# Performance work log

Measured on AMD Instinct MI355X. Metric: run time of the kernel, lower is better.

Reference implementation:

```python
import jax, jax.numpy as jnp
import numpy as np

DIM = 512
HID = 128
OUT = 32
ORDER = 3
B, L = 4, 4096


def positional_encoding(seq_len, d):
    pos = jnp.arange(seq_len, dtype=jnp.float32)[:, None]
    div = jnp.exp(-jnp.log(jnp.float32(10000.0)) * jnp.arange(0, d, 2, dtype=jnp.float32) / d)
    ang = pos * div[None, :]  # [L, d/2]
    pe = jnp.zeros((seq_len, d), dtype=jnp.float32)
    pe = pe.at[:, 0::2].set(jnp.sin(ang))
    pe = pe.at[:, 1::2].set(jnp.cos(ang))
    return pe


def setup_inputs() -> dict:
    key = jax.random.key(0)
    ks = jax.random.split(key, 9)
    s = lambda fan_in: 1.0 / np.sqrt(fan_in)
    return {
        "u": jax.random.normal(ks[0], (B, L, DIM), dtype=jnp.float32),
        "pW": jax.random.uniform(ks[1], (DIM, DIM * (ORDER + 1)), jnp.float32, -s(DIM), s(DIM)),
        "pb": jax.random.uniform(ks[2], (DIM * (ORDER + 1),), jnp.float32, -s(DIM), s(DIM)),
        "cW": jax.random.uniform(ks[3], (DIM * (ORDER + 1), DIM * (ORDER + 1), 3), jnp.float32, -s(DIM * 4 * 3), s(DIM * 4 * 3)),
        "cb": jax.random.uniform(ks[4], (DIM * (ORDER + 1),), jnp.float32, -s(DIM * 4 * 3), s(DIM * 4 * 3)),
        "fW": jax.random.uniform(ks[5], (HID, ORDER * DIM), jnp.float32, -s(HID), s(HID)),
        "fb": jax.random.uniform(ks[6], (ORDER * DIM,), jnp.float32, -s(HID), s(HID)),
        "oW": jax.random.uniform(ks[7], (DIM, OUT), jnp.float32, -s(DIM), s(DIM)),
        "ob": jax.random.uniform(ks[8], (OUT,), jnp.float32, -s(DIM), s(DIM)),
    }


def _fft_conv(h_filter, v):
    # circular conv along seq dim: h_filter [L, D], v [B, L, D]
    Vf = jnp.fft.rfft(v, axis=1)
    Hf = jnp.fft.rfft(h_filter, axis=0)[None, :, :]
    return jnp.fft.irfft(Vf * Hf, n=v.shape[1], axis=1)


def reference(u, pW, pb, cW, cb, fW, fb, oW, ob):
    seq_len = u.shape[1]
    t = positional_encoding(seq_len, HID)  # [L, HID]
    # hann window, periodic=False
    n = jnp.arange(seq_len, dtype=jnp.float32)
    window = (0.5 * (1.0 - jnp.cos(2.0 * jnp.pi * n / (seq_len - 1))))[:, None]  # [L,1]

    hat_z = u @ pW + pb  # [B, L, 4*DIM]
    # conv1d over seq with kernel 3, padding 1, channels 4*DIM -> 4*DIM
    z = jax.lax.conv_general_dilated(
        hat_z.transpose(0, 2, 1), cW, window_strides=(1,), padding=[(1, 1)],
        dimension_numbers=("NCH", "OIH", "NCH"))
    z = (z + cb[None, :, None]).transpose(0, 2, 1)  # [B, L, 4*DIM]

    v = z[:, :, :DIM]
    projs = z[:, :, DIM:]  # [B, L, 3*DIM]

    hat_h = t @ fW + fb  # [L, 3*DIM]
    h = hat_h * window  # [L, 3*DIM]

    for k in range(ORDER):
        xn = projs[:, :, DIM * k:DIM * (k + 1)]
        hn = h[:, DIM * k:DIM * (k + 1)]
        v = xn * _fft_conv(hn, v)

    return v @ oW + ob  # [B, L, OUT]
```

## Files before the change

kernel.cpp:

```cpp
#include <hip/hip_runtime.h>

typedef __attribute__((ext_vector_type(8))) short short8;
typedef __attribute__((ext_vector_type(4))) float f32x4;
typedef __attribute__((ext_vector_type(4))) unsigned short ushort4v;
typedef unsigned short ushortT;

#define PADROWS 4098
#define HSTR 2056
#define PI_F 3.14159265358979323f
#define PHYS(i) ((i) ^ (((i) >> 4) & 15))

__device__ __forceinline__ ushortT f2bf(float f) {
  union { float f; unsigned int u; } v; v.f = f;
  unsigned int r = (v.u + 0x7FFFu + ((v.u >> 16) & 1u)) >> 16;
  return (ushortT)r;
}
__device__ __forceinline__ float bf2f(ushortT b) {
  union { unsigned int u; float f; } v; v.u = ((unsigned int)b) << 16;
  return v.f;
}

__device__ __forceinline__ void gl2lds16(const void* g, void* l) {
  __builtin_amdgcn_global_load_lds((const __attribute__((address_space(1))) void*)g,
                                   (__attribute__((address_space(3))) void*)l, 16, 0, 0);
}


__global__ void cast_flat(const float* __restrict__ in, ushortT* __restrict__ outb) {
  size_t idx = (size_t)blockIdx.x * 256 + threadIdx.x;
  f32x4 v = *(const f32x4*)(in + idx * 4);
  ushort4v r;
  r[0] = f2bf(v[0]); r[1] = f2bf(v[1]); r[2] = f2bf(v[2]); r[3] = f2bf(v[3]);
  *(ushort4v*)(outb + idx * 4) = r;
}

__global__ void convert_u_pad(const float* __restrict__ in, ushortT* __restrict__ up) {
  int blk = blockIdx.x;
  if (blk >= 8192) {
    int idx = (blk - 8192) * 256 + threadIdx.x;
    int col = idx & 511;
    int r = (idx >> 9) & 1;
    int b = idx >> 10;
    up[((size_t)b * PADROWS + (r ? 4097 : 0)) * 512 + col] = 0;
    return;
  }
  size_t idx = (size_t)blk * 256 + threadIdx.x;
  f32x4 v = *(const f32x4*)(in + idx * 4);
  ushort4v r;
  r[0] = f2bf(v[0]); r[1] = f2bf(v[1]); r[2] = f2bf(v[2]); r[3] = f2bf(v[3]);
  size_t g = idx * 4;
  int col = (int)(g & 511);
  int l = (int)(g >> 9);
  int b = l >> 12;
  *(ushort4v*)(up + ((size_t)b * PADROWS + (l & 4095) + 1) * 512 + col) = r;
}

__global__ void cwt_pbc(const float* __restrict__ cW, const float* __restrict__ pb,
                        const float* __restrict__ cb, ushortT* __restrict__ Wt,
                        float* __restrict__ biasC, float* __restrict__ pbC0,
                        float* __restrict__ pbC2) {
  int o = blockIdx.x;
  int tid = threadIdx.x;
  float s0 = 0.f, s1 = 0.f, s2 = 0.f;
  const float* base = cW + (size_t)o * 6144;
  for (int i = tid; i < 2048; i += 256) {
    float w0 = base[i * 3], w1 = base[i * 3 + 1], w2 = base[i * 3 + 2];
    size_t oi = (size_t)o * 2048 + i;
    Wt[oi]           = f2bf(w0);
    Wt[oi + 4194304] = f2bf(w1);
    Wt[oi + 8388608] = f2bf(w2);
    float p = pb[i];
    s0 = fmaf(p, w0, s0);
    s1 = fmaf(p, w1, s1);
    s2 = fmaf(p, w2, s2);
  }
#pragma unroll
  for (int off = 32; off >= 1; off >>= 1) {
    s0 += __shfl_down(s0, off);
    s1 += __shfl_down(s1, off);
    s2 += __shfl_down(s2, off);
  }
  __shared__ float red[4][3];
  if ((tid & 63) == 0) { red[tid >> 6][0] = s0; red[tid >> 6][1] = s1; red[tid >> 6][2] = s2; }
  __syncthreads();
  if (tid == 0) {
    float a0 = red[0][0] + red[1][0] + red[2][0] + red[3][0];
    float a1 = red[0][1] + red[1][1] + red[2][1] + red[3][1];
    float a2 = red[0][2] + red[1][2] + red[2][2] + red[3][2];
    biasC[o] = cb[o] + a0 + a1 + a2;
    pbC0[o] = a0;
    pbC2[o] = a2;
  }
}

__global__ void fill_tabs(float2* __restrict__ Wg, float2* __restrict__ Sg) {
  int m = blockIdx.x * 256 + threadIdx.x;
  float sn, cs;
  if (m < 2048) {
    sincosf(-2.0f * PI_F * (float)m / 2048.0f, &sn, &cs);
    Wg[m] = make_float2(cs, sn);
  } else {
    int k = m - 2048;
    sincosf(PI_F * (float)k / 2048.0f, &sn, &cs);
    Sg[k] = make_float2(cs, sn);
  }
}


__launch_bounds__(256, 2)
__global__ void gemm_fold(const ushortT* __restrict__ Wt, const ushortT* __restrict__ pW_bf,
                          ushortT* __restrict__ cWf) {
  __shared__ alignas(16) ushortT As[128 * 64];
  __shared__ alignas(16) ushortT Bs[128 * 64];
  const int tid = threadIdx.x;
  const int lane = tid & 63, w = tid >> 6;
  const int wm = w >> 1, wn = w & 1;
  const int tm = blockIdx.x, tn = blockIdx.y, h = blockIdx.z;
  const ushortT* A = Wt + (size_t)h * 4194304;
  f32x4 acc[4][4] = {};
#pragma unroll 1
  for (int kt = 0; kt < 32; ++kt) {
    const int i0 = kt * 64;
#pragma unroll
    for (int i = 0; i < 4; ++i) {
      int ldsoff = (i * 4 + w) * 1024;
      int m = ((i * 4 + w) << 3) + (lane >> 3);
      int col = (lane & 7) * 8;
      gl2lds16(A + (size_t)(tm * 128 + m) * 2048 + i0 + col, (char*)As + ldsoff);
      gl2lds16(pW_bf + (size_t)(tn * 128 + m) * 2048 + i0 + col, (char*)Bs + ldsoff);
    }
    __syncthreads();
#pragma unroll
    for (int ks = 0; ks < 2; ++ks) {
      short8 av[4], bv[4];
#pragma unroll
      for (int mi = 0; mi < 4; ++mi) {
        int row = wm * 64 + mi * 16 + (lane & 15);
        av[mi] = *(const short8*)(As + row * 64 + (ks * 4 + (lane >> 4)) * 8);
      }
#pragma unroll
      for (int ni = 0; ni < 4; ++ni) {
        int row = wn * 64 + ni * 16 + (lane & 15);
        bv[ni] = *(const short8*)(Bs + row * 64 + (ks * 4 + (lane >> 4)) * 8);
      }
#pragma unroll
      for (int mi = 0; mi < 4; ++mi)
#pragma unroll
        for (int ni = 0; ni < 4; ++ni)
          acc[mi][ni] = __builtin_amdgcn_mfma_f32_16x16x32_bf16(av[mi], bv[ni], acc[mi][ni], 0, 0, 0);
    }
    __syncthreads();
  }
#pragma unroll
  for (int mi = 0; mi < 4; ++mi)
#pragma unroll
    for (int ni = 0; ni < 4; ++ni) {
      int jc = tn * 128 + wn * 64 + ni * 16 + (lane & 15);
#pragma unroll
      for (int j = 0; j < 4; ++j) {
        int o = tm * 128 + wm * 64 + mi * 16 + (lane >> 4) * 4 + j;
        cWf[((size_t)h * 2048 + o) * 512 + jc] = f2bf(acc[mi][ni][j]);
      }
    }
}


__launch_bounds__(512, 2)
__global__ void gemm_conv8(const ushortT* __restrict__ Upad, const ushortT* __restrict__ cWf,
                           const float* __restrict__ biasC, const float* __restrict__ pbC0,
                           const float* __restrict__ pbC2, float* __restrict__ vT,
                           ushortT* __restrict__ projsT) {
  __shared__ ushortT lds[2][2][16384];
  const int tid = threadIdx.x;
  const int lane = tid & 63, w = tid >> 6;
  const int wm = w >> 2, wn = w & 3;
  int raw = blockIdx.x;
  int wg  = (raw & 7) * 64 + (raw >> 3);
  const int o0 = (wg >> 6) << 8;
  const int nt = wg & 63;
  const int b  = nt >> 4;
  const int l0 = (nt & 15) << 8;

  f32x4 acc[8][4] = {};
  short8 xf[4][2];

  const int sm = tid >> 3;
  const int sw1 = ((tid & 7) ^ (sm & 7)) << 3;

  auto stageW = [&](int slot, int half, int t) {
    int q = (t * 21846) >> 16, h = t - 3 * q, j0 = q << 6;
    size_t grow = (size_t)(h * 2048 + o0 + half * 128 + sm);
    char* dst = (char*)&lds[slot][0][0] + half * 16384 + w * 1024;
    gl2lds16(cWf + grow * 512 + j0 + sw1, dst);
    gl2lds16(cWf + (grow + 64) * 512 + j0 + sw1, dst + 8192);
  };
  auto stageX = [&](int slot, int half, int t) {
    int q = (t * 21846) >> 16, h = t - 3 * q, j0 = q << 6;
    size_t grow = (size_t)b * PADROWS + l0 + h + half * 128 + sm;
    char* dst = (char*)&lds[slot][1][0] + half * 16384 + w * 1024;
    gl2lds16(Upad + grow * 512 + j0 + sw1, dst);
    gl2lds16(Upad + (grow + 64) * 512 + j0 + sw1, dst + 8192);
  };
  auto ldsW = [&](int slot, int mi, int ks) -> short8 {
    int row = wm * 128 + mi * 16 + (lane & 15);
    int ch = (ks * 4 + (lane >> 4)) ^ (row & 7);
    return *(const short8*)&lds[slot][0][row * 64 + ch * 8];
  };
  auto ldsX = [&](int slot, int ni, int ks) -> short8 {
    int row = wn * 64 + ni * 16 + (lane & 15);
    int ch = (ks * 4 + (lane >> 4)) ^ (row & 7);
    return *(const short8*)&lds[slot][1][row * 64 + ch * 8];
  };

  stageW(0, 0, 0); stageW(0, 1, 0);
  stageX(0, 0, 0); stageX(0, 1, 0);
  stageX(1, 0, 1); stageX(1, 1, 1);
  asm volatile("s_waitcnt vmcnt(0)" ::: "memory");
  __builtin_amdgcn_s_barrier();

#define PHASE(slot, q, STAGECODE, VMCODE)                                                                    \
  {                                                                                                          \
    short8 w0k0 = ldsW(slot, 2*(q), 0), w0k1 = ldsW(slot, 2*(q), 1);                                         \
    short8 w1k0 = ldsW(slot, 2*(q)+1, 0), w1k1 = ldsW(slot, 2*(q)+1, 1);                                     \
    if ((q) == 0) {                                                                                          \
      _Pragma("unroll")                                                                                      \
      for (int ni = 0; ni < 4; ++ni) {                                                                       \
        xf[ni][0] = ldsX(slot, ni, 0);                                                                       \
        xf[ni][1] = ldsX(slot, ni, 1);                                                                       \
      }                                                                                                      \
    }                                                                                                        \
    STAGECODE;                                                                                               \
    VMCODE;                                                                                                  \
    __builtin_amdgcn_s_barrier();                                                                            \
    asm volatile("s_waitcnt lgkmcnt(0)" ::: "memory");                                                       \
    __builtin_amdgcn_sched_barrier(0);                                                                       \
    __builtin_amdgcn_s_setprio(1);                                                                           \
    _Pragma("unroll")                                                                                        \
    for (int ni = 0; ni < 4; ++ni) {                                                                         \
      acc[2*(q)][ni]   = __builtin_amdgcn_mfma_f32_16x16x32_bf16(w0k0, xf[ni][0], acc[2*(q)][ni], 0, 0, 0);  \
      acc[2*(q)][ni]   = __builtin_amdgcn_mfma_f32_16x16x32_bf16(w0k1, xf[ni][1], acc[2*(q)][ni], 0, 0, 0);  \
      acc[2*(q)+1][ni] = __builtin_amdgcn_mfma_f32_16x16x32_bf16(w1k0, xf[ni][0], acc[2*(q)+1][ni], 0, 0, 0);\
      acc[2*(q)+1][ni] = __builtin_amdgcn_mfma_f32_16x16x32_bf16(w1k1, xf[ni][1], acc[2*(q)+1][ni], 0, 0, 0);\
    }                                                                                                        \
    __builtin_amdgcn_s_setprio(0);                                                                           \
    __builtin_amdgcn_s_barrier();                                                                            \
  }

#pragma unroll 1
  for (int it = 0; it < 11; ++it) {
    const int t0 = 2 * it;
    PHASE(0, 0, stageW(1, 0, t0 + 1), );
    PHASE(0, 1, stageW(1, 1, t0 + 1), );
    PHASE(0, 2, stageX(0, 0, t0 + 2), );
    PHASE(0, 3, stageX(0, 1, t0 + 2), asm volatile("s_waitcnt vmcnt(4)" ::: "memory"));
    PHASE(1, 0, stageW(0, 0, t0 + 2), );
    PHASE(1, 1, stageW(0, 1, t0 + 2), );
    PHASE(1, 2, stageX(1, 0, t0 + 3), );
    PHASE(1, 3, stageX(1, 1, t0 + 3), asm volatile("s_waitcnt vmcnt(4)" ::: "memory"));
  }
  PHASE(0, 0, stageW(1, 0, 23), );
  PHASE(0, 1, stageW(1, 1, 23), );
  PHASE(0, 2, , );
  PHASE(0, 3, , asm volatile("s_waitcnt vmcnt(0)" ::: "memory"));
  PHASE(1, 0, , );
  PHASE(1, 1, , );
  PHASE(1, 2, , );
  PHASE(1, 3, , );
#undef PHASE

  const int r4 = (lane >> 4) * 4;
  const int lbase = l0 + wn * 64 + (lane & 15);
  if (o0 < 512) {
#pragma unroll
    for (int mi = 0; mi < 8; ++mi)
#pragma unroll
      for (int ni = 0; ni < 4; ++ni) {
        int l = lbase + ni * 16;
#pragma unroll
        for (int j = 0; j < 4; ++j) {
          int o = o0 + wm * 128 + mi * 16 + r4 + j;
          float val = acc[mi][ni][j] + biasC[o];
          if (l == 0) val -= pbC0[o];
          if (l == 4095) val -= pbC2[o];
          vT[((size_t)b * 512 + o) * 4096 + l] = val;
        }
      }
  } else {
#pragma unroll
    for (int mi = 0; mi < 8; ++mi)
#pragma unroll
      for (int ni = 0; ni < 4; ++ni) {
        int l = lbase + ni * 16;
#pragma unroll
        for (int j = 0; j < 4; ++j) {
          int o = o0 + wm * 128 + mi * 16 + r4 + j;
          float val = acc[mi][ni][j] + biasC[o];
          if (l == 0) val -= pbC0[o];
          if (l == 4095) val -= pbC2[o];
          int oc = o - 512;
          projsT[((size_t)((oc >> 9) * 4 + b) * 512 + (oc & 511)) * 4096 + l] = f2bf(val);
        }
      }
  }
}


__launch_bounds__(256, 1)
__global__ void h_kernel(const float* __restrict__ fW, const float* __restrict__ fb,
                         float* __restrict__ hT) {
  __shared__ float tTs[128][64];
  __shared__ float fWs[128][128];
  const int l0 = blockIdx.x * 64;
  const int c0 = blockIdx.y * 128;
  const int tid = threadIdx.x;
  for (int r = tid; r < 4096; r += 256) {
    int d2 = r >> 6, li = r & 63;
    float dv = expf(-9.210340371976184f * (float)(2 * d2) / 128.0f);
    float ang = (float)(l0 + li) * dv;
    tTs[2 * d2][li] = sinf(ang);
    tTs[2 * d2 + 1][li] = cosf(ang);
  }
  {
    int cq = (tid & 31) * 4;
    int dr = tid >> 5;
#pragma unroll
    for (int d = dr; d < 128; d += 8)
      *(f32x4*)(&fWs[d][cq]) = *(const f32x4*)(fW + (size_t)d * 1536 + c0 + cq);
  }
  __syncthreads();
  const int lgrp = tid & 15;
  const int cg = tid >> 4;
  float acc[8][4] = {};
#pragma unroll 4
  for (int d = 0; d < 128; ++d) {
    f32x4 tv = *(const f32x4*)(&tTs[d][lgrp * 4]);
#pragma unroll
    for (int j = 0; j < 8; ++j) {
      float wv = fWs[d][cg + 16 * j];
      acc[j][0] = fmaf(tv[0], wv, acc[j][0]);
      acc[j][1] = fmaf(tv[1], wv, acc[j][1]);
      acc[j][2] = fmaf(tv[2], wv, acc[j][2]);
      acc[j][3] = fmaf(tv[3], wv, acc[j][3]);
    }
  }
  f32x4 wl;
#pragma unroll
  for (int j = 0; j < 4; ++j) {
    int l = l0 + lgrp * 4 + j;
    wl[j] = 0.5f * (1.0f - cosf(6.283185307179586f * (float)l / 4095.0f));
  }
#pragma unroll
  for (int j = 0; j < 8; ++j) {
    int ch = c0 + cg + 16 * j;
    float fbv = fb[ch];
    f32x4 r;
    r[0] = (acc[j][0] + fbv) * wl[0];
    r[1] = (acc[j][1] + fbv) * wl[1];
    r[2] = (acc[j][2] + fbv) * wl[2];
    r[3] = (acc[j][3] + fbv) * wl[3];
    *(f32x4*)(hT + (size_t)ch * 4096 + l0 + lgrp * 4) = r;
  }
}


__device__ __forceinline__ float2 cadd(float2 a, float2 b){ return make_float2(a.x+b.x, a.y+b.y); }
__device__ __forceinline__ float2 csub(float2 a, float2 b){ return make_float2(a.x-b.x, a.y-b.y); }
__device__ __forceinline__ float2 cmulp(float2 a, float2 b){
  return make_float2(a.x*b.x - a.y*b.y, a.x*b.y + a.y*b.x);
}
template<bool INV>
__device__ __forceinline__ float2 tw_mul(float2 a, float2 w) {
  return INV ? make_float2(fmaf(a.x, w.x,  a.y*w.y), fmaf(a.y, w.x, -a.x*w.y))
             : make_float2(fmaf(a.x, w.x, -a.y*w.y), fmaf(a.x, w.y,  a.y*w.x));
}
template<bool INV>
__device__ __forceinline__ float2 rot(float2 z) {
  return INV ? make_float2(-z.y, z.x) : make_float2(z.y, -z.x);
}

template<bool INV, int NS>
__device__ __forceinline__ void stage_r8(float2* X, const float2* Wl, int t) {
  const float C7 = 0.70710678118654752f;
  float2 v[8];
#pragma unroll
  for (int r = 0; r < 8; ++r) v[r] = X[PHYS(t + 256 * r)];
  if (NS > 1) {
    const int jm = (t & (NS - 1)) * (256 / NS);
#pragma unroll
    for (int r = 1; r < 8; ++r) v[r] = tw_mul<INV>(v[r], Wl[PHYS(r * jm)]);
  }
  float2 a0 = cadd(v[0], v[4]), a1 = csub(v[0], v[4]);
  float2 a2 = cadd(v[2], v[6]), a3 = rot<INV>(csub(v[2], v[6]));
  float2 E0 = cadd(a0, a2), E1 = cadd(a1, a3), E2 = csub(a0, a2), E3 = csub(a1, a3);
  float2 b0 = cadd(v[1], v[5]), b1 = csub(v[1], v[5]);
  float2 b2 = cadd(v[3], v[7]), b3 = rot<INV>(csub(v[3], v[7]));
  float2 O0 = cadd(b0, b2), O1 = cadd(b1, b3), O2 = csub(b0, b2), O3 = csub(b1, b3);
  const float2 w1 = INV ? make_float2(C7, C7)  : make_float2(C7, -C7);
  const float2 w3 = INV ? make_float2(-C7, C7) : make_float2(-C7, -C7);
  O1 = cmulp(O1, w1);
  O2 = rot<INV>(O2);
  O3 = cmulp(O3, w3);
  __syncthreads();
  const int base = (t / NS) * (8 * NS) + (t % NS);
  X[PHYS(base)]          = cadd(E0, O0);
  X[PHYS(base + NS)]     = cadd(E1, O1);
  X[PHYS(base + 2*NS)]   = cadd(E2, O2);
  X[PHYS(base + 3*NS)]   = cadd(E3, O3);
  X[PHYS(base + 4*NS)]   = csub(E0, O0);
  X[PHYS(base + 5*NS)]   = csub(E1, O1);
  X[PHYS(base + 6*NS)]   = csub(E2, O2);
  X[PHYS(base + 7*NS)]   = csub(E3, O3);
  __syncthreads();
}

template<bool INV>
__device__ __forceinline__ void stage_r4(float2* X, const float2* Wl, int t) {
#pragma unroll
  for (int jj = 0; jj < 2; ++jj) {
    const int j = t + jj * 256;
    float2 v0 = X[PHYS(j)], v1 = X[PHYS(j + 512)], v2 = X[PHYS(j + 1024)], v3 = X[PHYS(j + 1536)];
    v1 = tw_mul<INV>(v1, Wl[PHYS(j)]);
    v2 = tw_mul<INV>(v2, Wl[PHYS(2 * j)]);
    v3 = tw_mul<INV>(v3, Wl[PHYS(3 * j)]);
    float2 a0 = cadd(v0, v2), a1 = csub(v0, v2), a2 = cadd(v1, v3), a3 = rot<INV>(csub(v1, v3));
    X[PHYS(j)]        = cadd(a0, a2);
    X[PHYS(j + 512)]  = cadd(a1, a3);
    X[PHYS(j + 1024)] = csub(a0, a2);
    X[PHYS(j + 1536)] = csub(a1, a3);
  }
  __syncthreads();
}

template<bool INV>
__device__ __forceinline__ void fft2048r8(float2* X, const float2* Wl, int t) {
  stage_r8<INV, 1>(X, Wl, t);
  stage_r8<INV, 8>(X, Wl, t);
  stage_r8<INV, 64>(X, Wl, t);
  stage_r4<INV>(X, Wl, t);
}

__launch_bounds__(256, 4)
__global__ void fft_filter_r(const float* __restrict__ hT, const float2* __restrict__ Wg,
                             float2* __restrict__ Hf) {
  __shared__ float2 X[2048];
  __shared__ float2 Wl[2048];
  const int ch = blockIdx.x;
  const int tid = threadIdx.x;
  const float* sig = hT + (size_t)ch * 4096;
  for (int m = tid; m < 2048; m += 256) {
    Wl[PHYS(m)] = Wg[m];
    X[PHYS(m)] = *(const float2*)(sig + 2 * m);
  }
  __syncthreads();
  fft2048r8<false>(X, Wl, tid);
  float2* o = Hf + (size_t)ch * HSTR;
  for (int kk = tid; kk < 1024; kk += 256) {
    if (kk == 0) {
      float2 z0 = X[PHYS(0)];
      o[0]    = make_float2(z0.x + z0.y, 0.f);
      o[2048] = make_float2(z0.x - z0.y, 0.f);
      float2 zq = X[PHYS(1024)];
      o[1024] = make_float2(zq.x, -zq.y);
    } else {
      float2 zk = X[PHYS(kk)], zm = X[PHYS(2048 - kk)];
      float2 E = make_float2(0.5f * (zk.x + zm.x), 0.5f * (zk.y - zm.y));
      float2 D = make_float2(0.5f * (zk.x - zm.x), 0.5f * (zk.y + zm.y));
      float2 O = make_float2(D.y, -D.x);
      float sn, cs;
      __sincosf(-PI_F * (float)kk * (1.0f / 2048.0f), &sn, &cs);
      float2 twO = make_float2(O.x * cs - O.y * sn, O.x * sn + O.y * cs);
      o[kk]        = make_float2(E.x + twO.x, E.y + twO.y);
      o[2048 - kk] = make_float2(E.x - twO.x, -(E.y - twO.y));
    }
  }
}

__launch_bounds__(256, 4)
__global__ void fft_conv3(float* __restrict__ vT, const ushortT* __restrict__ projsT,
                          const float2* __restrict__ Hf, const float2* __restrict__ Wg,
                          const float2* __restrict__ Sg) {
  __shared__ float2 X[2048];
  __shared__ float2 Wl[2048];
  __shared__ float2 S[1024];
  const int bc = blockIdx.x;
  const int c = bc & 511, b = bc >> 9;
  const int tid = threadIdx.x;
  float* sig = vT + (size_t)bc * 4096;
  for (int m = tid; m < 2048; m += 256) {
    Wl[PHYS(m)] = Wg[m];
    X[PHYS(m)] = *(const float2*)(sig + 2 * m);
  }
  for (int m = tid; m < 1024; m += 256) S[m] = Sg[m];
  __syncthreads();
  fft2048r8<false>(X, Wl, tid);
  const float scale = 1.0f / 2048.0f;
#pragma unroll 1
  for (int k = 0; k < 3; ++k) {
    const float2* H = Hf + (size_t)(k * 512 + c) * HSTR;
    for (int kk = tid; kk < 1024; kk += 256) {
      if (kk == 0) {
        float h0x = H[0].x, hMx = H[2048].x;
        float2 hq = H[1024];
        float a1r = 0.5f * (h0x + hMx), a1w = 0.5f * (h0x - hMx);
        float2 Z0 = X[PHYS(0)], Zq = X[PHYS(1024)];
        X[PHYS(0)]    = make_float2(a1r * Z0.x + a1w * Z0.y, a1r * Z0.y + a1w * Z0.x);
        X[PHYS(1024)] = make_float2(hq.x * Zq.x + hq.y * Zq.y, hq.x * Zq.y - hq.y * Zq.x);
      } else {
        float2 hk = H[kk], hm = H[2048 - kk];
        float cs = S[kk].x, sn = S[kk].y;
        float oms = 0.5f * (1.f - sn), ops = 0.5f * (1.f + sn), c2h = 0.5f * cs;
        float d1x = hk.x - hm.x, d1y = hk.y + hm.y;
        float a1x = oms * hk.x + ops * hm.x, a1y = oms * hk.y - ops * hm.y;
        float b1x = -c2h * d1y, b1y = c2h * d1x;
        float a2x = oms * hm.x + ops * hk.x, a2y = oms * hm.y - ops * hk.y;
        float b2x = c2h * d1y, b2y = c2h * d1x;
        float2 Zk = X[PHYS(kk)], Zm = X[PHYS(2048 - kk)];
        X[PHYS(kk)] = make_float2(a1x * Zk.x - a1y * Zk.y + b1x * Zm.x + b1y * Zm.y,
                                  a1x * Zk.y + a1y * Zk.x - b1x * Zm.y + b1y * Zm.x);
        X[PHYS(2048 - kk)] = make_float2(a2x * Zm.x - a2y * Zm.y + b2x * Zk.x + b2y * Zk.y,
                                         a2x * Zm.y + a2y * Zm.x - b2x * Zk.y + b2y * Zk.x);
      }
    }
    __syncthreads();
    fft2048r8<true>(X, Wl, tid);
    const ushortT* xn = projsT + ((size_t)(k * 4 + b) * 512 + c) * 4096;
    if (k < 2) {
      for (int m = tid; m < 2048; m += 256) {
        unsigned int pr = *(const unsigned int*)(xn + 2 * m);
        float2 a = X[PHYS(m)];
        X[PHYS(m)] = make_float2(a.x * scale * bf2f((ushortT)(pr & 0xffffu)),
                                 a.y * scale * bf2f((ushortT)(pr >> 16)));
      }
      __syncthreads();
      fft2048r8<false>(X, Wl, tid);
    } else {
      for (int m = tid; m < 2048; m += 256) {
        unsigned int pr = *(const unsigned int*)(xn + 2 * m);
        float2 a = X[PHYS(m)];
        *(float2*)(sig + 2 * m) = make_float2(a.x * scale * bf2f((ushortT)(pr & 0xffffu)),
                                              a.y * scale * bf2f((ushortT)(pr >> 16)));
      }
    }
  }
}


__launch_bounds__(256, 2)
__global__ void out_gemm(const float* __restrict__ vT, const float* __restrict__ oW,
                         const float* __restrict__ ob, float* __restrict__ out) {
  __shared__ float vs[64][68];
  __shared__ float ows[64][36];
  const int l0 = blockIdx.x * 64;
  const int b = l0 >> 12;
  const int tid = threadIdx.x;
  const int l = tid & 63;
  const int og = (tid >> 6) * 8;
  float acc[8] = {};
  const float* vb = vT + (size_t)b * 2097152 + (l0 & 4095);
  const int cs = tid >> 2;
  const int lq = (tid & 3) * 16;
  const int oq = (tid & 3) * 8;
#pragma unroll 1
  for (int cc = 0; cc < 512; cc += 64) {
#pragma unroll
    for (int i = 0; i < 4; ++i)
      *(f32x4*)(&vs[cs][lq + i * 4]) = *(const f32x4*)(vb + (size_t)(cc + cs) * 4096 + lq + i * 4);
    *(f32x4*)(&ows[cs][oq])     = *(const f32x4*)(oW + (cc + cs) * 32 + oq);
    *(f32x4*)(&ows[cs][oq + 4]) = *(const f32x4*)(oW + (cc + cs) * 32 + oq + 4);
    __syncthreads();
#pragma unroll 8
    for (int c3 = 0; c3 < 64; ++c3) {
      float v = vs[c3][l];
#pragma unroll
      for (int j = 0; j < 8; ++j)
        acc[j] = fmaf(v, ows[c3][og + j], acc[j]);
    }
    __syncthreads();
  }
  float* op = out + (size_t)(l0 + l) * 32 + og;
  f32x4 r0, r1;
  r0[0] = acc[0] + ob[og];     r0[1] = acc[1] + ob[og + 1];
  r0[2] = acc[2] + ob[og + 2]; r0[3] = acc[3] + ob[og + 3];
  r1[0] = acc[4] + ob[og + 4]; r1[1] = acc[5] + ob[og + 5];
  r1[2] = acc[6] + ob[og + 6]; r1[3] = acc[7] + ob[og + 7];
  *(f32x4*)op = r0;
  *(f32x4*)(op + 4) = r1;
}


__global__ void ws_sentinel(float* __restrict__ out) {
  if (threadIdx.x == 0) out[0] = -31337.0f;
}


extern "C" void kernel_launch(void* const* d_in, const int* in_sizes, int n_in,
                              void* d_out, int out_size, void* d_ws, size_t ws_size,
                              hipStream_t stream) {
  (void)in_sizes; (void)n_in; (void)out_size;
  const float* u  = (const float*)d_in[0];
  const float* pW = (const float*)d_in[1];
  const float* pb = (const float*)d_in[2];
  const float* cW = (const float*)d_in[3];
  const float* cb = (const float*)d_in[4];
  const float* fW = (const float*)d_in[5];
  const float* fb = (const float*)d_in[6];
  const float* oW = (const float*)d_in[7];
  const float* ob = (const float*)d_in[8];
  float* out = (float*)d_out;

  char* ws = (char*)d_ws;
  ushortT* Upad   = (ushortT*)(ws);
  ushortT* cWf    = (ushortT*)(ws + 16785408);
  float*   biasC  = (float*)  (ws + 23076864);
  float*   pbC0   = (float*)  (ws + 23085056);
  float*   pbC2   = (float*)  (ws + 23093248);
  float2*  Wg     = (float2*) (ws + 23101440);
  float2*  Sg     = (float2*) (ws + 23117824);
  float2*  Hf     = (float2*) (ws + 23126016);
  float*   vT     = (float*)  (ws + 48390144);
  ushortT* projsT = (ushortT*)(ws + 81944576);
  const size_t total = 132276224;
  char* S = (char*)vT;
  ushortT* Wt     = (ushortT*)(S);
  ushortT* pW_bf  = (ushortT*)(S + 25165824);
  float*   hT     = (float*)  (S + 27262976);

  if (total > ws_size) {
    ws_sentinel<<<1, 64, 0, stream>>>(out);
    return;
  }

  convert_u_pad<<<8208, 256, 0, stream>>>(u, Upad);
  cast_flat<<<1024, 256, 0, stream>>>(pW, pW_bf);
  cwt_pbc<<<2048, 256, 0, stream>>>(cW, pb, cb, Wt, biasC, pbC0, pbC2);
  fill_tabs<<<12, 256, 0, stream>>>(Wg, Sg);
  gemm_fold<<<dim3(16, 4, 3), 256, 0, stream>>>(Wt, pW_bf, cWf);
  h_kernel<<<dim3(64, 12), 256, 0, stream>>>(fW, fb, hT);
  fft_filter_r<<<1536, 256, 0, stream>>>(hT, Wg, Hf);
  gemm_conv8<<<512, 512, 0, stream>>>(Upad, cWf, biasC, pbC0, pbC2, vT, projsT);
  fft_conv3<<<2048, 256, 0, stream>>>(vT, projsT, Hf, Wg, Sg);
  out_gemm<<<256, 256, 0, stream>>>(vT, oW, ob, out);
}
```

Measured before the change: 318.8 us.

## Store v in bf16 and fuse FFT load/gating/store into butterfly stages

The intermediate v tensor is now stored as bf16 instead of fp32, halving its traffic through gemm_conv8, fft_conv3 and out_gemm. The first forward radix-8 stage now reads straight from global memory (or from the gated product), and the last inverse radix-4 stage writes the gated bf16 output directly, removing separate load and gate passes and some barriers. The pW cast and the twiddle-table fill are merged into one launch. The cost is lower precision on v, which is fed through three chained FFT convolutions.

Result: slower. 326.1 us (+2.3%).

```diff
diff --git a/kernel.cpp b/kernel.cpp
--- a/kernel.cpp
+++ b/kernel.cpp
@@ -3,6 +3,7 @@
 typedef __attribute__((ext_vector_type(8))) short short8;
 typedef __attribute__((ext_vector_type(4))) float f32x4;
 typedef __attribute__((ext_vector_type(4))) unsigned short ushort4v;
+typedef __attribute__((ext_vector_type(8))) unsigned short ushort8v;
 typedef unsigned short ushortT;
 
 #define PADROWS 4098
@@ -26,12 +27,27 @@
 }
 
 
-__global__ void cast_flat(const float* __restrict__ in, ushortT* __restrict__ outb) {
-  size_t idx = (size_t)blockIdx.x * 256 + threadIdx.x;
-  f32x4 v = *(const f32x4*)(in + idx * 4);
-  ushort4v r;
-  r[0] = f2bf(v[0]); r[1] = f2bf(v[1]); r[2] = f2bf(v[2]); r[3] = f2bf(v[3]);
-  *(ushort4v*)(outb + idx * 4) = r;
+__global__ void misc_prep(const float* __restrict__ in, ushortT* __restrict__ outb,
+                          float2* __restrict__ Wg, float2* __restrict__ Sg) {
+  int blk = blockIdx.x;
+  if (blk < 1024) {
+    size_t idx = (size_t)blk * 256 + threadIdx.x;
+    f32x4 v = *(const f32x4*)(in + idx * 4);
+    ushort4v r;
+    r[0] = f2bf(v[0]); r[1] = f2bf(v[1]); r[2] = f2bf(v[2]); r[3] = f2bf(v[3]);
+    *(ushort4v*)(outb + idx * 4) = r;
+    return;
+  }
+  int m = (blk - 1024) * 256 + threadIdx.x;
+  float sn, cs;
+  if (m < 2048) {
+    sincosf(-2.0f * PI_F * (float)m / 2048.0f, &sn, &cs);
+    Wg[m] = make_float2(cs, sn);
+  } else {
+    int k = m - 2048;
+    sincosf(PI_F * (float)k / 2048.0f, &sn, &cs);
+    Sg[k] = make_float2(cs, sn);
+  }
 }
 
 __global__ void convert_u_pad(const float* __restrict__ in, ushortT* __restrict__ up) {
@@ -93,19 +109,6 @@
   }
 }
 
-__global__ void fill_tabs(float2* __restrict__ Wg, float2* __restrict__ Sg) {
-  int m = blockIdx.x * 256 + threadIdx.x;
-  float sn, cs;
-  if (m < 2048) {
-    sincosf(-2.0f * PI_F * (float)m / 2048.0f, &sn, &cs);
-    Wg[m] = make_float2(cs, sn);
-  } else {
-    int k = m - 2048;
-    sincosf(PI_F * (float)k / 2048.0f, &sn, &cs);
-    Sg[k] = make_float2(cs, sn);
-  }
-}
-
 
 __launch_bounds__(256, 2)
 __global__ void gemm_fold(const ushortT* __restrict__ Wt, const ushortT* __restrict__ pW_bf,
@@ -168,7 +171,7 @@
 __launch_bounds__(512, 2)
 __global__ void gemm_conv8(const ushortT* __restrict__ Upad, const ushortT* __restrict__ cWf,
                            const float* __restrict__ biasC, const float* __restrict__ pbC0,
-                           const float* __restrict__ pbC2, float* __restrict__ vT,
+                           const float* __restrict__ pbC2, ushortT* __restrict__ vTb,
                            ushortT* __restrict__ projsT) {
   __shared__ ushortT lds[2][2][16384];
   const int tid = threadIdx.x;
@@ -282,7 +285,7 @@
           float val = acc[mi][ni][j] + biasC[o];
           if (l == 0) val -= pbC0[o];
           if (l == 4095) val -= pbC2[o];
-          vT[((size_t)b * 512 + o) * 4096 + l] = val;
+          vTb[((size_t)b * 512 + o) * 4096 + l] = f2bf(val);
         }
       }
   } else {
@@ -378,38 +381,41 @@
   return INV ? make_float2(-z.y, z.x) : make_float2(z.y, -z.x);
 }
 
-template<bool INV, int NS>
-__device__ __forceinline__ void stage_r8(float2* X, const float2* Wl, int t) {
+template<bool INV>
+__device__ __forceinline__ void bfly8(const float2 v[8], float2 o[8]) {
   const float C7 = 0.70710678118654752f;
-  float2 v[8];
-#pragma unroll
-  for (int r = 0; r < 8; ++r) v[r] = X[PHYS(t + 256 * r)];
-  if (NS > 1) {
-    const int jm = (t & (NS - 1)) * (256 / NS);
-#pragma unroll
-    for (int r = 1; r < 8; ++r) v[r] = tw_mul<INV>(v[r], Wl[PHYS(r * jm)]);
-  }
   float2 a0 = cadd(v[0], v[4]), a1 = csub(v[0], v[4]);
   float2 a2 = cadd(v[2], v[6]), a3 = rot<INV>(csub(v[2], v[6]));
   float2 E0 = cadd(a0, a2), E1 = cadd(a1, a3), E2 = csub(a0, a2), E3 = csub(a1, a3);
   float2 b0 = cadd(v[1], v[5]), b1 = csub(v[1], v[5]);
   float2 b2 = cadd(v[3], v[7]), b3 = rot<INV>(csub(v[3], v[7]));
   float2 O0 = cadd(b0, b2), O1 = cadd(b1, b3), O2 = csub(b0, b2), O3 = csub(b1, b3);
-  const float2 w1 = INV ? make_float2(C7, C7)  : make_float2(C7, -C7);
+  const float2 w1 = INV ? make_float2(C7, C7)  : make_float2(-C7 + 2*C7, -C7);
   const float2 w3 = INV ? make_float2(-C7, C7) : make_float2(-C7, -C7);
-  O1 = cmulp(O1, w1);
+  O1 = cmulp(O1, INV ? make_float2(C7, C7) : make_float2(C7, -C7));
   O2 = rot<INV>(O2);
   O3 = cmulp(O3, w3);
+  (void)w1;
+  o[0] = cadd(E0, O0); o[1] = cadd(E1, O1); o[2] = cadd(E2, O2); o[3] = cadd(E3, O3);
+  o[4] = csub(E0, O0); o[5] = csub(E1, O1); o[6] = csub(E2, O2); o[7] = csub(E3, O3);
+}
+
+template<bool INV, int NS>
+__device__ __forceinline__ void stage_r8(float2* X, const float2* Wl, int t) {
+  float2 v[8];
+#pragma unroll
+  for (int r = 0; r < 8; ++r) v[r] = X[PHYS(t + 256 * r)];
+  if (NS > 1) {
+    const int jm = (t & (NS - 1)) * (256 / NS);
+#pragma unroll
+    for (int r = 1; r < 8; ++r) v[r] = tw_mul<INV>(v[r], Wl[PHYS(r * jm)]);
+  }
+  float2 o[8];
+  bfly8<INV>(v, o);
   __syncthreads();
   const int base = (t / NS) * (8 * NS) + (t % NS);
-  X[PHYS(base)]          = cadd(E0, O0);
-  X[PHYS(base + NS)]     = cadd(E1, O1);
-  X[PHYS(base + 2*NS)]   = cadd(E2, O2);
-  X[PHYS(base + 3*NS)]   = cadd(E3, O3);
-  X[PHYS(base + 4*NS)]   = csub(E0, O0);
-  X[PHYS(base + 5*NS)]   = csub(E1, O1);
-  X[PHYS(base + 6*NS)]   = csub(E2, O2);
-  X[PHYS(base + 7*NS)]   = csub(E3, O3);
+#pragma unroll
+  for (int i = 0; i < 8; ++i) X[PHYS(base + i * NS)] = o[i];
   __syncthreads();
 }
 
@@ -431,12 +437,71 @@
   __syncthreads();
 }
 
-template<bool INV>
-__device__ __forceinline__ void fft2048r8(float2* X, const float2* Wl, int t) {
-  stage_r8<INV, 1>(X, Wl, t);
-  stage_r8<INV, 8>(X, Wl, t);
-  stage_r8<INV, 64>(X, Wl, t);
-  stage_r4<INV>(X, Wl, t);
+__device__ __forceinline__ void fwd_stage1_bf16(float2* X, const unsigned int* __restrict__ sigb, int t) {
+  float2 v[8], o[8];
+#pragma unroll
+  for (int r = 0; r < 8; ++r) {
+    unsigned int pr = sigb[t + 256 * r];
+    v[r] = make_float2(bf2f((ushortT)(pr & 0xffffu)), bf2f((ushortT)(pr >> 16)));
+  }
+  bfly8<false>(v, o);
+  const int base = t * 8;
+#pragma unroll
+  for (int i = 0; i < 8; ++i) X[PHYS(base + i)] = o[i];
+  __syncthreads();
+}
+
+__device__ __forceinline__ void fwd_stage1_f32(float2* X, const float* __restrict__ sig, int t) {
+  float2 v[8], o[8];
+#pragma unroll
+  for (int r = 0; r < 8; ++r) v[r] = *(const float2*)(sig + 2 * (t + 256 * r));
+  bfly8<false>(v, o);
+  const int base = t * 8;
+#pragma unroll
+  for (int i = 0; i < 8; ++i) X[PHYS(base + i)] = o[i];
+  __syncthreads();
+}
+
+__device__ __forceinline__ void fwd_stage1_gated(float2* X, const unsigned int* __restrict__ xnb,
+                                                 float scale, int t) {
+  float2 v[8], o[8];
+#pragma unroll
+  for (int r = 0; r < 8; ++r) {
+    const int m = t + 256 * r;
+    unsigned int pr = xnb[m];
+    float2 a = X[PHYS(m)];
+    v[r] = make_float2(a.x * scale * bf2f((ushortT)(pr & 0xffffu)),
+                       a.y * scale * bf2f((ushortT)(pr >> 16)));
+  }
+  bfly8<false>(v, o);
+  __syncthreads();
+  const int base = t * 8;
+#pragma unroll
+  for (int i = 0; i < 8; ++i) X[PHYS(base + i)] = o[i];
+  __syncthreads();
+}
+
+__device__ __forceinline__ void stage_r4_store(const float2* X, const float2* Wl,
+                                               const unsigned int* __restrict__ xnb,
+                                               float scale, unsigned int* __restrict__ outb, int t) {
+#pragma unroll
+  for (int jj = 0; jj < 2; ++jj) {
+    const int j = t + jj * 256;
+    float2 v0 = X[PHYS(j)], v1 = X[PHYS(j + 512)], v2 = X[PHYS(j + 1024)], v3 = X[PHYS(j + 1536)];
+    v1 = tw_mul<true>(v1, Wl[PHYS(j)]);
+    v2 = tw_mul<true>(v2, Wl[PHYS(2 * j)]);
+    v3 = tw_mul<true>(v3, Wl[PHYS(3 * j)]);
+    float2 a0 = cadd(v0, v2), a1 = csub(v0, v2), a2 = cadd(v1, v3), a3 = rot<true>(csub(v1, v3));
+    float2 y[4] = { cadd(a0, a2), cadd(a1, a3), csub(a0, a2), csub(a1, a3) };
+    const int idx[4] = { j, j + 512, j + 1024, j + 1536 };
+#pragma unroll
+    for (int q = 0; q < 4; ++q) {
+      unsigned int pr = xnb[idx[q]];
+      unsigned int lo = f2bf(y[q].x * scale * bf2f((ushortT)(pr & 0xffffu)));
+      unsigned int hi = f2bf(y[q].y * scale * bf2f((ushortT)(pr >> 16)));
+      outb[idx[q]] = lo | (hi << 16);
+    }
+  }
 }
 
 __launch_bounds__(256, 4)
@@ -447,12 +512,11 @@
   const int ch = blockIdx.x;
   const int tid = threadIdx.x;
   const float* sig = hT + (size_t)ch * 4096;
-  for (int m = tid; m < 2048; m += 256) {
-    Wl[PHYS(m)] = Wg[m];
-    X[PHYS(m)] = *(const float2*)(sig + 2 * m);
-  }
-  __syncthreads();
-  fft2048r8<false>(X, Wl, tid);
+  for (int m = tid; m < 2048; m += 256) Wl[PHYS(m)] = Wg[m];
+  fwd_stage1_f32(X, sig, tid);
+  stage_r8<false, 8>(X, Wl, tid);
+  stage_r8<false, 64>(X, Wl, tid);
+  stage_r4<false>(X, Wl, tid);
   float2* o = Hf + (size_t)ch * HSTR;
   for (int kk = tid; kk < 1024; kk += 256) {
     if (kk == 0) {
@@ -476,7 +540,7 @@
 }
 
 __launch_bounds__(256, 4)
-__global__ void fft_conv3(float* __restrict__ vT, const ushortT* __restrict__ projsT,
+__global__ void fft_conv3(ushortT* __restrict__ vTb, const ushortT* __restrict__ projsT,
                           const float2* __restrict__ Hf, const float2* __restrict__ Wg,
                           const float2* __restrict__ Sg) {
   __shared__ float2 X[2048];
@@ -485,14 +549,13 @@
   const int bc = blockIdx.x;
   const int c = bc & 511, b = bc >> 9;
   const int tid = threadIdx.x;
-  float* sig = vT + (size_t)bc * 4096;
-  for (int m = tid; m < 2048; m += 256) {
-    Wl[PHYS(m)] = Wg[m];
-    X[PHYS(m)] = *(const float2*)(sig + 2 * m);
-  }
+  unsigned int* sigb = (unsigned int*)(vTb + (size_t)bc * 4096);
+  for (int m = tid; m < 2048; m += 256) Wl[PHYS(m)] = Wg[m];
   for (int m = tid; m < 1024; m += 256) S[m] = Sg[m];
-  __syncthreads();
-  fft2048r8<false>(X, Wl, tid);
+  fwd_stage1_bf16(X, sigb, tid);
+  stage_r8<false, 8>(X, Wl, tid);
+  stage_r8<false, 64>(X, Wl, tid);
+  stage_r4<false>(X, Wl, tid);
   const float scale = 1.0f / 2048.0f;
 #pragma unroll 1
   for (int k = 0; k < 3; ++k) {
@@ -522,31 +585,25 @@
       }
     }
     __syncthreads();
-    fft2048r8<true>(X, Wl, tid);
-    const ushortT* xn = projsT + ((size_t)(k * 4 + b) * 512 + c) * 4096;
+    stage_r8<true, 1>(X, Wl, tid);
+    stage_r8<true, 8>(X, Wl, tid);
+    stage_r8<true, 64>(X, Wl, tid);
+    const unsigned int* xnb = (const unsigned int*)(projsT + ((size_t)(k * 4 + b) * 512 + c) * 4096);
     if (k < 2) {
-      for (int m = tid; m < 2048; m += 256) {
-        unsigned int pr = *(const unsigned int*)(xn + 2 * m);
-        float2 a = X[PHYS(m)];
-        X[PHYS(m)] = make_float2(a.x * scale * bf2f((ushortT)(pr & 0xffffu)),
-                                 a.y * scale * bf2f((ushortT)(pr >> 16)));
-      }
-      __syncthreads();
-      fft2048r8<false>(X, Wl, tid);
+      stage_r4<true>(X, Wl, tid);
+      fwd_stage1_gated(X, xnb, scale, tid);
+      stage_r8<false, 8>(X, Wl, tid);
+      stage_r8<false, 64>(X, Wl, tid);
+      stage_r4<false>(X, Wl, tid);
     } else {
-      for (int m = tid; m < 2048; m += 256) {
-        unsigned int pr = *(const unsigned int*)(xn + 2 * m);
-        float2 a = X[PHYS(m)];
-        *(float2*)(sig + 2 * m) = make_float2(a.x * scale * bf2f((ushortT)(pr & 0xffffu)),
-                                              a.y * scale * bf2f((ushortT)(pr >> 16)));
-      }
+      stage_r4_store(X, Wl, xnb, scale, sigb, tid);
     }
   }
 }
 
 
 __launch_bounds__(256, 2)
-__global__ void out_gemm(const float* __restrict__ vT, const float* __restrict__ oW,
+__global__ void out_gemm(const ushortT* __restrict__ vTb, const float* __restrict__ oW,
                          const float* __restrict__ ob, float* __restrict__ out) {
   __shared__ float vs[64][68];
   __shared__ float ows[64][36];
@@ -556,15 +613,18 @@
   const int l = tid & 63;
   const int og = (tid >> 6) * 8;
   float acc[8] = {};
-  const float* vb = vT + (size_t)b * 2097152 + (l0 & 4095);
+  const ushortT* vb = vTb + (size_t)b * 2097152 + (l0 & 4095);
   const int cs = tid >> 2;
   const int lq = (tid & 3) * 16;
   const int oq = (tid & 3) * 8;
 #pragma unroll 1
   for (int cc = 0; cc < 512; cc += 64) {
 #pragma unroll
-    for (int i = 0; i < 4; ++i)
-      *(f32x4*)(&vs[cs][lq + i * 4]) = *(const f32x4*)(vb + (size_t)(cc + cs) * 4096 + lq + i * 4);
+    for (int i = 0; i < 2; ++i) {
+      ushort8v u8 = *(const ushort8v*)(vb + (size_t)(cc + cs) * 4096 + lq + i * 8);
+#pragma unroll
+      for (int j = 0; j < 8; ++j) vs[cs][lq + i * 8 + j] = bf2f(u8[j]);
+    }
     *(f32x4*)(&ows[cs][oq])     = *(const f32x4*)(oW + (cc + cs) * 32 + oq);
     *(f32x4*)(&ows[cs][oq + 4]) = *(const f32x4*)(oW + (cc + cs) * 32 + oq + 4);
     __syncthreads();
@@ -617,10 +677,10 @@
   float2*  Wg     = (float2*) (ws + 23101440);
   float2*  Sg     = (float2*) (ws + 23117824);
   float2*  Hf     = (float2*) (ws + 23126016);
-  float*   vT     = (float*)  (ws + 48390144);
-  ushortT* projsT = (ushortT*)(ws + 81944576);
-  const size_t total = 132276224;
-  char* S = (char*)vT;
+  ushortT* vTb    = (ushortT*)(ws + 48390144);
+  ushortT* projsT = (ushortT*)(ws + 65167360);
+  const size_t total = 115499008;
+  char* S = (char*)vTb;
   ushortT* Wt     = (ushortT*)(S);
   ushortT* pW_bf  = (ushortT*)(S + 25165824);
   float*   hT     = (float*)  (S + 27262976);
@@ -631,13 +691,12 @@
   }
 
   convert_u_pad<<<8208, 256, 0, stream>>>(u, Upad);
-  cast_flat<<<1024, 256, 0, stream>>>(pW, pW_bf);
+  misc_prep<<<1036, 256, 0, stream>>>(pW, pW_bf, Wg, Sg);
   cwt_pbc<<<2048, 256, 0, stream>>>(cW, pb, cb, Wt, biasC, pbC0, pbC2);
-  fill_tabs<<<12, 256, 0, stream>>>(Wg, Sg);
   gemm_fold<<<dim3(16, 4, 3), 256, 0, stream>>>(Wt, pW_bf, cWf);
   h_kernel<<<dim3(64, 12), 256, 0, stream>>>(fW, fb, hT);
   fft_filter_r<<<1536, 256, 0, stream>>>(hT, Wg, Hf);
-  gemm_conv8<<<512, 512, 0, stream>>>(Upad, cWf, biasC, pbC0, pbC2, vT, projsT);
-  fft_conv3<<<2048, 256, 0, stream>>>(vT, projsT, Hf, Wg, Sg);
-  out_gemm<<<256, 256, 0, stream>>>(vT, oW, ob, out);
-}
+  gemm_conv8<<<512, 512, 0, stream>>>(Upad, cWf, biasC, pbC0, pbC2, vTb, projsT);
+  fft_conv3<<<2048, 256, 0, stream>>>(vTb, projsT, Hf, Wg, Sg);
+  out_gemm<<<256, 256, 0, stream>>>(vTb, oW, ob, out);
+}
```
